# Kernel tuning notes

Measured on AMD Instinct MI355X. Metric: run time of the kernel, lower is better.

Reference implementation:

```python
import jax, jax.numpy as jnp
import numpy as np

EMBED_DIM = 768
HIDDEN_DIM = 384          # max(embed_dim // 2, 128)
NUM_HEADS = 12
HEAD_DIM = EMBED_DIM // NUM_HEADS
LAYER_VOCAB = 4           # len(target_layers)
THRESHOLD = 0.5
MIN_KEEP_RATIO = 0.1
B, N = 8, 1024


def setup_inputs() -> dict:
    key = jax.random.key(0)
    ks = jax.random.split(key, 12)
    std = 0.02
    return {
        "tokens": jax.random.normal(ks[0], (B, N, EMBED_DIM), jnp.float32),
        "layer_token_idx": 1,
        # actor params
        "layer_emb": jax.random.normal(ks[1], (LAYER_VOCAB, EMBED_DIM), jnp.float32) * std,
        "ln_g": jnp.ones((EMBED_DIM,), jnp.float32),
        "ln_b": jnp.zeros((EMBED_DIM,), jnp.float32),
        "w1": jax.random.normal(ks[2], (HIDDEN_DIM, EMBED_DIM), jnp.float32) * std,
        "b1": jnp.zeros((HIDDEN_DIM,), jnp.float32),
        "w2": jax.random.normal(ks[3], (HIDDEN_DIM, HIDDEN_DIM), jnp.float32) * std,
        "b2": jnp.zeros((HIDDEN_DIM,), jnp.float32),
        "w3": jax.random.normal(ks[4], (1, HIDDEN_DIM), jnp.float32) * std,
        "b3": jnp.zeros((1,), jnp.float32),
        # attention params (timm-style)
        "qkv_w": jax.random.normal(ks[5], (3 * EMBED_DIM, EMBED_DIM), jnp.float32) * std,
        "qkv_b": jnp.zeros((3 * EMBED_DIM,), jnp.float32),
        "proj_w": jax.random.normal(ks[6], (EMBED_DIM, EMBED_DIM), jnp.float32) * std,
        "proj_b": jnp.zeros((EMBED_DIM,), jnp.float32),
    }


def _layernorm(x, g, b, eps=1e-5):
    mu = x.mean(-1, keepdims=True)
    var = ((x - mu) ** 2).mean(-1, keepdims=True)
    return (x - mu) * jax.lax.rsqrt(var + eps) * g + b


def _forward(tokens, layer_token_idx, layer_emb, ln_g, ln_b, w1, b1, w2, b2, w3, b3,
             qkv_w, qkv_b, proj_w, proj_b):
    Bsz, Ntok, C = tokens.shape
    # --- MAPPOActor: logits ---
    ctx = tokens + layer_emb[layer_token_idx]               # broadcast [C]
    ctx = ctx + ctx.mean(axis=1, keepdims=True)             # global context
    h = _layernorm(ctx, ln_g, ln_b)
    h = jax.nn.gelu(h @ w1.T + b1, approximate=False)
    h = jax.nn.gelu(h @ w2.T + b2, approximate=False)
    logits = (h @ w3.T + b3).squeeze(-1)                    # [B, N]
    probs = jax.nn.sigmoid(logits)
    # --- compute_mask: threshold + min-keep topk correction ---
    binary = probs >= THRESHOLD                             # [B, N] bool
    min_keep = max(int(Ntok * MIN_KEEP_RATIO), 1)
    min_keep = min(min_keep, Ntok)
    _, topk_idx = jax.lax.top_k(probs, min_keep)            # [B, min_keep]
    fixed = jnp.zeros((Bsz, Ntok), bool).at[jnp.arange(Bsz)[:, None], topk_idx].set(True)
    need_fix = binary.sum(-1) < min_keep                    # [B]
    mask = jnp.where(need_fix[:, None], fixed, binary)
    mask = mask.at[:, 0].set(True)
    # --- masked attention (timm style) ---
    qkv = tokens @ qkv_w.T + qkv_b                          # [B, N, 3C]
    qkv = qkv.reshape(Bsz, Ntok, 3, NUM_HEADS, HEAD_DIM).transpose(2, 0, 3, 1, 4)
    q, k, v = qkv[0], qkv[1], qkv[2]                        # [B, H, N, D]
    q = q * (HEAD_DIM ** -0.5)
    scores = jnp.einsum("bhnd,bhmd->bhnm", q, k)            # [B, H, N, N]
    neg = jnp.finfo(scores.dtype).min
    scores = jnp.where(mask[:, None, None, :], scores, neg)
    attn = jax.nn.softmax(scores, axis=-1)
    v = v * mask[:, None, :, None].astype(v.dtype)
    out = jnp.einsum("bhnm,bhmd->bhnd", attn, v)
    out = out.transpose(0, 2, 1, 3).reshape(Bsz, Ntok, C)
    out = out @ proj_w.T + proj_b
    out = out * mask[..., None].astype(out.dtype)           # zero_out_queries=True
    return out


def reference(tokens, layer_token_idx, layer_emb, ln_g, ln_b, w1, b1, w2, b2, w3, b3,
              qkv_w, qkv_b, proj_w, proj_b):
    return _forward(tokens, layer_token_idx, layer_emb, ln_g, ln_b, w1, b1, w2, b2,
                    w3, b3, qkv_w, qkv_b, proj_w, proj_b)
```

## Files before the change

### kernel.cpp

```cpp
#include <hip/hip_runtime.h>
#include <cstdint>
#include <cmath>

#define EMBED 768
#define HID 384
#define NHEAD 12
#define HDIM 64
#define BATCH 8
#define NTOK 1024
#define MINKEEP 102

using f32x4  = __attribute__((ext_vector_type(4))) float;
using short8 = __attribute__((ext_vector_type(8))) short;
using short4v = __attribute__((ext_vector_type(4))) short;
using half8  = __attribute__((ext_vector_type(8))) _Float16;

__device__ inline short f2bf(float f) {
  unsigned u = __float_as_uint(f);
  u += 0x7fffu + ((u >> 16) & 1u);
  return (short)(u >> 16);
}
__device__ inline float bf2f(short s) {
  return __uint_as_float(((unsigned)(unsigned short)s) << 16);
}
__device__ inline unsigned pack_bf2(float lo, float hi) {
  unsigned ul = __float_as_uint(lo);
  ul += 0x7fffu + ((ul >> 16) & 1u);
  unsigned uh = __float_as_uint(hi);
  uh += 0x7fffu + ((uh >> 16) & 1u);
  return (ul >> 16) | (uh & 0xffff0000u);
}
__device__ inline void split2h(float v, short& h, short& m) {
  _Float16 h0 = (_Float16)v;
  float r = v - (float)h0;
  _Float16 m0 = (_Float16)r;
  h = __builtin_bit_cast(short, h0);
  m = __builtin_bit_cast(short, m0);
}

__global__ __launch_bounds__(256) void prep_kernel(
    const float* __restrict__ qkv_w, short* __restrict__ wq_bf,
    const float* __restrict__ proj_w, short* __restrict__ wp_bf,
    const float* __restrict__ w1, short* __restrict__ w1h, short* __restrict__ w1m,
    const float* __restrict__ w2, short* __restrict__ w2h, short* __restrict__ w2m,
    const float* __restrict__ tokens, float* __restrict__ colsum,
    float* __restrict__ lgt) {
  int blk = blockIdx.x, tid = threadIdx.x;
  if (blk < 2304) {
    const float* in = (blk < 1728) ? qkv_w : proj_w;
    short* out = (blk < 1728) ? wq_bf : wp_bf;
    int i = (blk < 1728 ? blk : blk - 1728) * 256 + tid;
    float4 f = ((const float4*)in)[i];
    short4v s;
    s[0] = f2bf(f.x); s[1] = f2bf(f.y); s[2] = f2bf(f.z); s[3] = f2bf(f.w);
    ((short4v*)out)[i] = s;
  } else if (blk < 2736) {
    const float* in = (blk < 2592) ? w1 : w2;
    short* oh = (blk < 2592) ? w1h : w2h;
    short* om = (blk < 2592) ? w1m : w2m;
    int i = (blk < 2592 ? blk - 2304 : blk - 2592) * 256 + tid;
    float4 f = ((const float4*)in)[i];
    short4v h, m;
    short th, tm;
    split2h(f.x, th, tm); h[0] = th; m[0] = tm;
    split2h(f.y, th, tm); h[1] = th; m[1] = tm;
    split2h(f.z, th, tm); h[2] = th; m[2] = tm;
    split2h(f.w, th, tm); h[3] = th; m[3] = tm;
    ((short4v*)oh)[i] = h;
    ((short4v*)om)[i] = m;
  } else if (blk < 2744) {
    int i = (blk - 2736) * 256 + tid;
    ((float4*)lgt)[i] = make_float4(0.f, 0.f, 0.f, 0.f);
  } else {
    int idx = blk - 2744;
    int b = idx >> 4, chunk = idx & 15;
    const float* tb = tokens + ((size_t)b * NTOK + chunk * 64) * EMBED;
    float s0 = 0.f, s1 = 0.f, s2 = 0.f;
#pragma unroll 8
    for (int n = 0; n < 64; ++n) {
      const float* r = tb + (size_t)n * EMBED;
      s0 += r[tid]; s1 += r[tid + 256]; s2 += r[tid + 512];
    }
    atomicAdd(&colsum[b * EMBED + tid], s0);
    atomicAdd(&colsum[b * EMBED + tid + 256], s1);
    atomicAdd(&colsum[b * EMBED + tid + 512], s2);
  }
}

__global__ __launch_bounds__(256) void ln_split_kernel(
    const float* __restrict__ tokens, const float* __restrict__ colsum,
    const float* __restrict__ layer_emb, const int* __restrict__ lidx,
    const float* __restrict__ gamma, const float* __restrict__ beta,
    short* __restrict__ xh, short* __restrict__ xm,
    short* __restrict__ tok_bf) {
  int row = blockIdx.x;
  int b = row >> 10;
  __shared__ float s_row[EMBED];
  __shared__ float s_red[4];
  const float* tr = tokens + (size_t)row * EMBED;
  const float* cs = colsum + b * EMBED;
  const float* eb = layer_emb + lidx[0] * EMBED;
  float lsum = 0.f;
  for (int c = threadIdx.x; c < EMBED; c += 256) {
    float t = tr[c];
    tok_bf[(size_t)row * EMBED + c] = f2bf(t);
    float v = t + 2.0f * eb[c] + cs[c] * (1.0f / NTOK);
    s_row[c] = v;
    lsum += v;
  }
  for (int o = 32; o; o >>= 1) lsum += __shfl_down(lsum, o, 64);
  int wid = threadIdx.x >> 6;
  if ((threadIdx.x & 63) == 0) s_red[wid] = lsum;
  __syncthreads();
  float mu = (s_red[0] + s_red[1] + s_red[2] + s_red[3]) * (1.f / EMBED);
  float lss = 0.f;
  for (int c = threadIdx.x; c < EMBED; c += 256) {
    float d = s_row[c] - mu;
    lss += d * d;
  }
  for (int o = 32; o; o >>= 1) lss += __shfl_down(lss, o, 64);
  __syncthreads();
  if ((threadIdx.x & 63) == 0) s_red[wid] = lss;
  __syncthreads();
  float var = (s_red[0] + s_red[1] + s_red[2] + s_red[3]) * (1.f / EMBED);
  float rinv = 1.0f / sqrtf(var + 1e-5f);
  for (int c = threadIdx.x; c < EMBED; c += 256) {
    float v = (s_row[c] - mu) * rinv * gamma[c] + beta[c];
    short h, m;
    split2h(v, h, m);
    size_t idx = (size_t)row * EMBED + c;
    xh[idx] = h; xm[idx] = m;
  }
}

__device__ inline float gelu_exact(float x) {
  return 0.5f * x * (1.0f + erff(x * 0.70710678118654752f));
}

template <int OUT>
__global__ __launch_bounds__(256) void gemm_split_kernel(
    const short* __restrict__ Ah, const short* __restrict__ Am,
    const short* __restrict__ Wh, const short* __restrict__ Wm,
    const float* __restrict__ bias, short* __restrict__ Ch,
    short* __restrict__ Cm, const float* __restrict__ w3,
    float* __restrict__ lgt, int M, int N, int K) {
  __shared__ short sA[2][64][40];
  __shared__ short sW[2][64][40];
  int tid = threadIdx.x;
  int w = tid >> 6, l = tid & 63, lg = l >> 4, lb = l & 15;
  int wr = (w >> 1) * 32, wc = (w & 1) * 32;
  int row0 = blockIdx.x * 64, col0 = blockIdx.y * 64;
  int srow = tid >> 2;
  int skk = (tid & 3) * 8;
  f32x4 acc0[2][2] = {}, acc1[2][2] = {};
  short8 ra0, ra1, rw0, rw1;
  {
    size_t aoff = (size_t)(row0 + srow) * K + skk;
    size_t woff = (size_t)(col0 + srow) * K + skk;
    ra0 = *(const short8*)(Ah + aoff);
    ra1 = *(const short8*)(Am + aoff);
    rw0 = *(const short8*)(Wh + woff);
    rw1 = *(const short8*)(Wm + woff);
  }
  for (int k0 = 0; k0 < K; k0 += 32) {
    __syncthreads();
    *(short8*)&sA[0][srow][skk] = ra0;
    *(short8*)&sA[1][srow][skk] = ra1;
    *(short8*)&sW[0][srow][skk] = rw0;
    *(short8*)&sW[1][srow][skk] = rw1;
    __syncthreads();
    if (k0 + 32 < K) {
      size_t aoff = (size_t)(row0 + srow) * K + k0 + 32 + skk;
      size_t woff = (size_t)(col0 + srow) * K + k0 + 32 + skk;
      ra0 = *(const short8*)(Ah + aoff);
      ra1 = *(const short8*)(Am + aoff);
      rw0 = *(const short8*)(Wh + woff);
      rw1 = *(const short8*)(Wm + woff);
    }
    half8 ah[2], am[2], bh[2], bm[2];
#pragma unroll
    for (int i = 0; i < 2; ++i) {
      ah[i] = *(half8*)&sA[0][wr + i * 16 + lb][lg * 8];
      am[i] = *(half8*)&sA[1][wr + i * 16 + lb][lg * 8];
      bh[i] = *(half8*)&sW[0][wc + i * 16 + lb][lg * 8];
      bm[i] = *(half8*)&sW[1][wc + i * 16 + lb][lg * 8];
    }
#pragma unroll
    for (int i = 0; i < 2; ++i)
#pragma unroll
      for (int j = 0; j < 2; ++j) {
        f32x4 c0 = acc0[i][j];
        f32x4 c1 = acc1[i][j];
        c0 = __builtin_amdgcn_mfma_f32_16x16x32_f16(ah[i], bh[j], c0, 0, 0, 0);
        c1 = __builtin_amdgcn_mfma_f32_16x16x32_f16(ah[i], bm[j], c1, 0, 0, 0);
        c0 = __builtin_amdgcn_mfma_f32_16x16x32_f16(am[i], bh[j], c0, 0, 0, 0);
        acc0[i][j] = c0;
        acc1[i][j] = c1;
      }
  }
  if (OUT == 0) {
#pragma unroll
    for (int i = 0; i < 2; ++i) {
#pragma unroll
      for (int j = 0; j < 2; ++j) {
#pragma unroll
        for (int r = 0; r < 4; ++r) {
          int grow = row0 + wr + i * 16 + lg * 4 + r;
          int gcol = col0 + wc + j * 16 + lb;
          float g = gelu_exact(acc0[i][j][r] + acc1[i][j][r] + bias[gcol]);
          size_t idx = (size_t)grow * N + gcol;
          short h, m;
          split2h(g, h, m);
          Ch[idx] = h; Cm[idx] = m;
        }
      }
    }
  } else {
    float part[2][4];
#pragma unroll
    for (int i = 0; i < 2; ++i)
#pragma unroll
      for (int r = 0; r < 4; ++r) part[i][r] = 0.f;
#pragma unroll
    for (int i = 0; i < 2; ++i) {
#pragma unroll
      for (int j = 0; j < 2; ++j) {
#pragma unroll
        for (int r = 0; r < 4; ++r) {
          int gcol = col0 + wc + j * 16 + lb;
          float g = gelu_exact(acc0[i][j][r] + acc1[i][j][r] + bias[gcol]);
          part[i][r] += g * w3[gcol];
        }
      }
    }
#pragma unroll
    for (int i = 0; i < 2; ++i) {
#pragma unroll
      for (int r = 0; r < 4; ++r) {
        float v = part[i][r];
        v += __shfl_xor(v, 1);
        v += __shfl_xor(v, 2);
        v += __shfl_xor(v, 4);
        v += __shfl_xor(v, 8);
        if (lb == 0) atomicAdd(&lgt[row0 + wr + i * 16 + lg * 4 + r], v);
      }
    }
  }
}

__global__ __launch_bounds__(1024) void mask_kernel(
    const float* __restrict__ lgt, const float* __restrict__ b3,
    int* __restrict__ kidx, int* __restrict__ kc, float* __restrict__ biasc) {
  int b = blockIdx.x, tid = threadIdx.x;
  __shared__ unsigned long long keys[1024];
  __shared__ int flag[1024];
  __shared__ int wsum[16];
  float v = lgt[b * NTOK + tid] + b3[0];
  bool bin = (v >= 0.0f);
  int wid = tid >> 6, lane = tid & 63;
  unsigned long long bal = __ballot(bin);
  if (lane == 0) wsum[wid] = __popcll(bal);
  __syncthreads();
  int total = 0;
  for (int q = 0; q < 16; ++q) total += wsum[q];
  int mv;
  if (total >= MINKEEP) {
    mv = bin ? 1 : 0;
  } else {
    flag[tid] = 0;
    unsigned u = __float_as_uint(v);
    u = (u & 0x80000000u) ? ~u : (u | 0x80000000u);
    keys[tid] = ((unsigned long long)u << 32) | (unsigned)(1023 - tid);
    __syncthreads();
    for (int k2 = 2; k2 <= 1024; k2 <<= 1) {
      for (int j = k2 >> 1; j > 0; j >>= 1) {
        int ixj = tid ^ j;
        if (ixj > tid) {
          unsigned long long a = keys[tid], c = keys[ixj];
          bool desc = ((tid & k2) == 0);
          if (desc ? (a < c) : (a > c)) {
            keys[tid] = c;
            keys[ixj] = a;
          }
        }
        __syncthreads();
      }
    }
    if (tid < MINKEEP) {
      int idx = 1023 - (int)(keys[tid] & 0xFFFFFFFFu);
      flag[idx] = 1;
    }
    __syncthreads();
    mv = flag[tid];
  }
  if (tid == 0) mv = 1;
  __syncthreads();
  unsigned long long fb = __ballot(mv != 0);
  if (lane == 0) wsum[wid] = __popcll(fb);
  __syncthreads();
  int base = 0, tot = 0;
  for (int q = 0; q < 16; ++q) {
    int vq = wsum[q];
    if (q < wid) base += vq;
    tot += vq;
  }
  if (mv) {
    int pre = base + __popcll(fb & ((1ull << lane) - 1ull));
    kidx[b * NTOK + pre] = tid;
    biasc[b * NTOK + pre] = 0.f;
  } else {
    int nbase = wid * 64 - base;
    int npre = nbase + __popcll(~fb & ((1ull << lane) - 1ull));
    kidx[b * NTOK + tot + npre] = tid;
    biasc[b * NTOK + tot + npre] = -3.0e38f;
  }
  if (tid == 0) kc[b] = tot;
}

__global__ __launch_bounds__(256) void qkv_gather_kernel(
    const short* __restrict__ tok_bf, const short* __restrict__ W,
    const float* __restrict__ bias, const int* __restrict__ kidx,
    const int* __restrict__ kc, short* __restrict__ qq,
    short* __restrict__ kk_, short* __restrict__ VTc) {
  __shared__ short smem[(64 + 128) * 72];
  short (*sA)[72] = (short(*)[72])smem;
  short (*sW)[72] = (short(*)[72])(smem + 64 * 72);
  __shared__ int s_idx[64];
  int bx = blockIdx.x;
  int b = bx & 7, bt = bx >> 3;
  int kcb = kc[b];
  if (bt * 64 >= kcb) return;
  int tid = threadIdx.x;
  if (tid < 64) s_idx[tid] = kidx[b * NTOK + bt * 64 + tid];
  int w = tid >> 6, l = tid & 63, lg = l >> 4, lb = l & 15;
  int wr = (w >> 1) * 32, wc = (w & 1) * 64;
  int col0 = blockIdx.y * 128;
  int r_ = tid >> 3, kq = (tid & 7) * 8;
  __syncthreads();
  const short* Ab = tok_bf + (size_t)b * NTOK * EMBED;
  f32x4 acc[2][4] = {};
  short8 pa[2], pw[4];
#pragma unroll
  for (int t = 0; t < 2; ++t)
    pa[t] = *(const short8*)(Ab + (size_t)s_idx[t * 32 + r_] * EMBED + kq);
#pragma unroll
  for (int t = 0; t < 4; ++t)
    pw[t] = *(const short8*)(W + (size_t)(col0 + t * 32 + r_) * EMBED + kq);
  for (int k0 = 0; k0 < EMBED; k0 += 64) {
    __syncthreads();
#pragma unroll
    for (int t = 0; t < 2; ++t) *(short8*)&sA[t * 32 + r_][kq] = pa[t];
#pragma unroll
    for (int t = 0; t < 4; ++t) *(short8*)&sW[t * 32 + r_][kq] = pw[t];
    __syncthreads();
    if (k0 + 64 < EMBED) {
#pragma unroll
      for (int t = 0; t < 2; ++t)
        pa[t] = *(const short8*)(Ab + (size_t)s_idx[t * 32 + r_] * EMBED +
                                 k0 + 64 + kq);
#pragma unroll
      for (int t = 0; t < 4; ++t)
        pw[t] = *(const short8*)(W + (size_t)(col0 + t * 32 + r_) * EMBED +
                                 k0 + 64 + kq);
    }
#pragma unroll
    for (int half = 0; half < 2; ++half) {
      short8 af[2], bfr[4];
#pragma unroll
      for (int i = 0; i < 2; ++i)
        af[i] = *(short8*)&sA[wr + i * 16 + lb][half * 32 + lg * 8];
#pragma unroll
      for (int j = 0; j < 4; ++j)
        bfr[j] = *(short8*)&sW[wc + j * 16 + lb][half * 32 + lg * 8];
#pragma unroll
      for (int i = 0; i < 2; ++i)
#pragma unroll
        for (int j = 0; j < 4; ++j)
          acc[i][j] = __builtin_amdgcn_mfma_f32_16x16x32_bf16(af[i], bfr[j],
                                                              acc[i][j], 0, 0, 0);
    }
  }
  if (col0 >= 2 * EMBED) {
    __syncthreads();
    short (*sT)[72] = (short(*)[72])smem;
#pragma unroll
    for (int i = 0; i < 2; ++i) {
#pragma unroll
      for (int j = 0; j < 4; ++j) {
        int col_local = wc + j * 16 + lb;
        int jr0 = wr + i * 16 + lg * 4;
        short4v v4;
#pragma unroll
        for (int r = 0; r < 4; ++r)
          v4[r] = f2bf(acc[i][j][r] + bias[col0 + col_local]);
        *(short4v*)&sT[col_local][jr0] = v4;
      }
    }
    __syncthreads();
    int rem = col0 - 2 * EMBED;
#pragma unroll
    for (int t = 0; t < 4; ++t) {
      int c = tid + t * 256;
      int rowl = c >> 3;
      int off = (c & 7) * 8;
      int vcol = rem + rowl;
      int h = vcol >> 6, d = vcol & 63;
      size_t dst = ((size_t)(b * NHEAD + h) * HDIM + d) * NTOK + bt * 64 + off;
      *(short8*)(VTc + dst) = *(short8*)&sT[rowl][off];
    }
    return;
  }
#pragma unroll
  for (int i = 0; i < 2; ++i) {
#pragma unroll
    for (int j = 0; j < 4; ++j) {
#pragma unroll
      for (int r = 0; r < 4; ++r) {
        int jrow = bt * 64 + wr + i * 16 + lg * 4 + r;
        int gcol = col0 + wc + j * 16 + lb;
        float val = acc[i][j][r] + bias[gcol];
        int which = gcol / EMBED;
        int rem2 = gcol - which * EMBED;
        int h = rem2 >> 6, d = rem2 & 63;
        size_t dst = ((size_t)(b * NHEAD + h) * NTOK + jrow) * HDIM + d;
        if (which == 0)
          qq[dst] = f2bf(val * 0.125f);
        else
          kk_[dst] = f2bf(val);
      }
    }
  }
}

#define ATTN_SWZ(row, colbyte) (((row)*128) + ((colbyte) ^ (((row)&7) << 4)))

__global__ __launch_bounds__(256) void attn_mfma3_kernel(
    const short* __restrict__ Qc, const short* __restrict__ Kc,
    const short* __restrict__ VTc, const float* __restrict__ biasc,
    const int* __restrict__ kc, short* __restrict__ ao) {
  __shared__ __align__(16) short sK[64 * 64];
  __shared__ __align__(16) short sVT[64 * 64];
  int bid = blockIdx.x;
  int xcd = bid & 7, slot = bid >> 3;
  int bh = xcd * 12 + (slot >> 4);
  int qt = slot & 15;
  int b = bh / NHEAD;
  int kcb = kc[b];
  if (qt * 64 >= kcb) return;
  int nt = (kcb + 63) >> 6;
  int tid = threadIdx.x;
  int w = tid >> 6, l = tid & 63, lg = l >> 4, lb = l & 15;
  int n0 = qt * 64 + w * 16;
  const short* Qp = Qc + ((size_t)bh * NTOK + n0) * HDIM;
  const short* Kp = Kc + (size_t)bh * NTOK * HDIM;
  const short* Vp = VTc + (size_t)bh * HDIM * NTOK;
  const float* bp = biasc + b * NTOK;

  short8 qf[2];
#pragma unroll
  for (int hh = 0; hh < 2; ++hh)
    qf[hh] = *(const short8*)(Qp + lb * HDIM + hh * 32 + lg * 8);

  f32x4 acc[4] = {};
  float lr = 0.f;

  int srow = tid >> 3;
  int scol = (tid & 7) * 8;
  int scolb = scol * 2;
  short8 rk0, rk1, rv0, rv1;

#define ATTN_LOADT(m0_)                                                        \
  {                                                                            \
    rk0 = *(const short8*)(Kp + (size_t)((m0_) + srow) * HDIM + scol);         \
    rk1 = *(const short8*)(Kp + (size_t)((m0_) + srow + 32) * HDIM + scol);    \
    rv0 = *(const short8*)(Vp + (size_t)srow * NTOK + (m0_) + scol);           \
    rv1 = *(const short8*)(Vp + (size_t)(srow + 32) * NTOK + (m0_) + scol);    \
  }

  ATTN_LOADT(0);
  for (int t = 0; t < nt; ++t) {
    int m0 = t * 64;
    *(short8*)((char*)sK + ATTN_SWZ(srow, scolb)) = rk0;
    *(short8*)((char*)sK + ATTN_SWZ(srow + 32, scolb)) = rk1;
    *(short8*)((char*)sVT + ATTN_SWZ(srow, scolb)) = rv0;
    *(short8*)((char*)sVT + ATTN_SWZ(srow + 32, scolb)) = rv1;
    __syncthreads();
    if (t + 1 < nt) ATTN_LOADT(m0 + 64);

    f32x4 bias4[4];
#pragma unroll
    for (int s = 0; s < 4; ++s)
      bias4[s] = *(const f32x4*)(bp + m0 + s * 16 + lg * 4);

    f32x4 S[4];
#pragma unroll
    for (int s = 0; s < 4; ++s) {
      short8 kf0 = *(const short8*)((const char*)sK +
                                    ATTN_SWZ(s * 16 + lb, lg * 16));
      short8 kf1 = *(const short8*)((const char*)sK +
                                    ATTN_SWZ(s * 16 + lb, 64 + lg * 16));
      f32x4 c = bias4[s];
      c = __builtin_amdgcn_mfma_f32_16x16x32_bf16(kf0, qf[0], c, 0, 0, 0);
      c = __builtin_amdgcn_mfma_f32_16x16x32_bf16(kf1, qf[1], c, 0, 0, 0);
      S[s] = c;
    }

    unsigned pk[4][2];
    {
      float rs = 0.f;
#pragma unroll
      for (int s = 0; s < 4; ++s) {
        float p0 = __expf(S[s][0]);
        float p1 = __expf(S[s][1]);
        float p2 = __expf(S[s][2]);
        float p3 = __expf(S[s][3]);
        rs += (p0 + p1) + (p2 + p3);
        pk[s][0] = pack_bf2(p0, p1);
        pk[s][1] = pack_bf2(p2, p3);
      }
      rs += __shfl_xor(rs, 16);
      rs += __shfl_xor(rs, 32);
      lr += rs;
    }

    bool hi = (lg & 2) != 0;
    int srcl = ((lg & 1) * 2) * 16 + lb;
#pragma unroll
    for (int t2 = 0; t2 < 2; ++t2) {
      short8 vf[4];
#pragma unroll
      for (int u = 0; u < 4; ++u)
        vf[u] = *(const short8*)((const char*)sVT +
                                 ATTN_SWZ(u * 16 + lb, t2 * 64 + lg * 16));
      int a0 = __shfl((int)pk[2 * t2][0], srcl);
      int b0 = __shfl((int)pk[2 * t2 + 1][0], srcl);
      int a1 = __shfl((int)pk[2 * t2][1], srcl);
      int b1 = __shfl((int)pk[2 * t2 + 1][1], srcl);
      int a2 = __shfl((int)pk[2 * t2][0], srcl + 16);
      int b2 = __shfl((int)pk[2 * t2 + 1][0], srcl + 16);
      int a3 = __shfl((int)pk[2 * t2][1], srcl + 16);
      int b3 = __shfl((int)pk[2 * t2 + 1][1], srcl + 16);
      union { short8 s8; int u[4]; } pa;
      pa.u[0] = hi ? b0 : a0;
      pa.u[1] = hi ? b1 : a1;
      pa.u[2] = hi ? b2 : a2;
      pa.u[3] = hi ? b3 : a3;
#pragma unroll
      for (int u = 0; u < 4; ++u)
        acc[u] = __builtin_amdgcn_mfma_f32_16x16x32_bf16(pa.s8, vf[u],
                                                         acc[u], 0, 0, 0);
    }
    __syncthreads();
  }

  int h = bh - b * NHEAD;
#pragma unroll
  for (int r = 0; r < 4; ++r) {
    float inv = 1.0f / __shfl(lr, lg * 4 + r);
    int j = n0 + lg * 4 + r;
#pragma unroll
    for (int u = 0; u < 4; ++u) {
      ao[((size_t)b * NTOK + j) * EMBED + h * HDIM + u * 16 + lb] =
          f2bf(acc[u][r] * inv);
    }
  }
}

__global__ __launch_bounds__(256) void proj_gather_kernel(
    const short* __restrict__ A, const short* __restrict__ W,
    const float* __restrict__ bias, const int* __restrict__ kidx,
    const int* __restrict__ kc, float* __restrict__ out) {
  __shared__ short sA[64][72];
  __shared__ short sW[128][72];
  __shared__ int s_idx[64];
  int bx = blockIdx.x;
  int b = bx & 7, bt = bx >> 3;
  int kcb = kc[b];
  int tid = threadIdx.x;
  if (tid < 64) s_idx[tid] = kidx[b * NTOK + bt * 64 + tid];
  int col0 = blockIdx.y * 128;
  if (bt * 64 >= kcb) {
    __syncthreads();
#pragma unroll
    for (int t = 0; t < 8; ++t) {
      int c = tid + t * 256;
      int rowl = c >> 5;
      int c4 = c & 31;
      int n = s_idx[rowl];
      ((float4*)(out + ((size_t)b * NTOK + n) * EMBED + col0))[c4] =
          make_float4(0.f, 0.f, 0.f, 0.f);
    }
    return;
  }
  int w = tid >> 6, l = tid & 63, lg = l >> 4, lb = l & 15;
  int wr = (w >> 1) * 32, wc = (w & 1) * 64;
  int r_ = tid >> 3, kq = (tid & 7) * 8;
  const short* Ab = A + ((size_t)b * NTOK + bt * 64) * EMBED;
  f32x4 acc[2][4] = {};
  short8 pa[2], pw[4];
  __syncthreads();
#pragma unroll
  for (int t = 0; t < 2; ++t)
    pa[t] = *(const short8*)(Ab + (size_t)(t * 32 + r_) * EMBED + kq);
#pragma unroll
  for (int t = 0; t < 4; ++t)
    pw[t] = *(const short8*)(W + (size_t)(col0 + t * 32 + r_) * EMBED + kq);
  for (int k0 = 0; k0 < EMBED; k0 += 64) {
    __syncthreads();
#pragma unroll
    for (int t = 0; t < 2; ++t) *(short8*)&sA[t * 32 + r_][kq] = pa[t];
#pragma unroll
    for (int t = 0; t < 4; ++t) *(short8*)&sW[t * 32 + r_][kq] = pw[t];
    __syncthreads();
    if (k0 + 64 < EMBED) {
#pragma unroll
      for (int t = 0; t < 2; ++t)
        pa[t] = *(const short8*)(Ab + (size_t)(t * 32 + r_) * EMBED + k0 + 64 + kq);
#pragma unroll
      for (int t = 0; t < 4; ++t)
        pw[t] = *(const short8*)(W + (size_t)(col0 + t * 32 + r_) * EMBED + k0 + 64 + kq);
    }
#pragma unroll
    for (int half = 0; half < 2; ++half) {
      short8 af[2], bfr[4];
#pragma unroll
      for (int i = 0; i < 2; ++i)
        af[i] = *(short8*)&sA[wr + i * 16 + lb][half * 32 + lg * 8];
#pragma unroll
      for (int j = 0; j < 4; ++j)
        bfr[j] = *(short8*)&sW[wc + j * 16 + lb][half * 32 + lg * 8];
#pragma unroll
      for (int i = 0; i < 2; ++i)
#pragma unroll
        for (int j = 0; j < 4; ++j)
          acc[i][j] = __builtin_amdgcn_mfma_f32_16x16x32_bf16(af[i], bfr[j],
                                                              acc[i][j], 0, 0, 0);
    }
  }
#pragma unroll
  for (int i = 0; i < 2; ++i) {
#pragma unroll
    for (int j = 0; j < 4; ++j) {
#pragma unroll
      for (int r = 0; r < 4; ++r) {
        int jloc = wr + i * 16 + lg * 4 + r;
        int jrow = bt * 64 + jloc;
        int gcol = col0 + wc + j * 16 + lb;
        int n = s_idx[jloc];
        out[((size_t)b * NTOK + n) * EMBED + gcol] =
            (jrow < kcb) ? (acc[i][j][r] + bias[gcol]) : 0.f;
      }
    }
  }
}

extern "C" void kernel_launch(void* const* d_in, const int* in_sizes, int n_in,
                              void* d_out, int out_size, void* d_ws, size_t ws_size,
                              hipStream_t stream) {
  const float* tokens   = (const float*)d_in[0];
  const int*   lidx     = (const int*)d_in[1];
  const float* layer_emb= (const float*)d_in[2];
  const float* ln_g     = (const float*)d_in[3];
  const float* ln_b     = (const float*)d_in[4];
  const float* w1       = (const float*)d_in[5];
  const float* b1       = (const float*)d_in[6];
  const float* w2       = (const float*)d_in[7];
  const float* b2       = (const float*)d_in[8];
  const float* w3       = (const float*)d_in[9];
  const float* b3       = (const float*)d_in[10];
  const float* qkv_w    = (const float*)d_in[11];
  const float* qkv_b    = (const float*)d_in[12];
  const float* proj_w   = (const float*)d_in[13];
  const float* proj_b   = (const float*)d_in[14];
  float* out = (float*)d_out;
  float* ws = (float*)d_ws;

  float* colsum = ws;
  float* lgt    = ws + 6144;
  int*   kidx   = (int*)(ws + 14336);
  float* biasc  = ws + 22528;
  int*   kc     = (int*)(ws + 30720);
  short* tok_bf = (short*)(ws + 30736);
  short* wq_bf  = (short*)(ws + 3176464);
  short* wp_bf  = (short*)(ws + 4061200);
  short* w1h = (short*)(ws + 4356112);
  short* w1m = (short*)(ws + 4503568);
  short* w2h = (short*)(ws + 4798480);
  short* w2m = (short*)(ws + 4872208);
  const size_t X0 = 5019664;
  short* xh  = (short*)(ws + X0);
  short* xm  = (short*)(ws + X0 + 3145728);
  short* h1h = (short*)(ws + X0 + 9437184);
  short* h1m = (short*)(ws + X0 + 11010048);
  short* Qc   = (short*)(ws + X0);
  short* Kc   = (short*)(ws + X0 + 3145728);
  short* VTc  = (short*)(ws + X0 + 9437184);
  short* aoc  = (short*)(ws + X0 + 12582912);

  hipMemsetAsync(colsum, 0, BATCH * EMBED * sizeof(float), stream);

  prep_kernel<<<dim3(2872), dim3(256), 0, stream>>>(
      qkv_w, wq_bf, proj_w, wp_bf, w1, w1h, w1m, w2, w2h, w2m,
      tokens, colsum, lgt);

  ln_split_kernel<<<dim3(BATCH * NTOK), dim3(256), 0, stream>>>(
      tokens, colsum, layer_emb, lidx, ln_g, ln_b, xh, xm, tok_bf);
  gemm_split_kernel<0><<<dim3(128, 6), dim3(256), 0, stream>>>(
      xh, xm, w1h, w1m, b1, h1h, h1m, nullptr, nullptr,
      BATCH * NTOK, HID, EMBED);
  gemm_split_kernel<1><<<dim3(128, 6), dim3(256), 0, stream>>>(
      h1h, h1m, w2h, w2m, b2, nullptr, nullptr, w3, lgt,
      BATCH * NTOK, HID, HID);
  mask_kernel<<<dim3(BATCH), dim3(1024), 0, stream>>>(lgt, b3, kidx, kc, biasc);

  qkv_gather_kernel<<<dim3(128, 18), dim3(256), 0, stream>>>(
      tok_bf, wq_bf, qkv_b, kidx, kc, Qc, Kc, VTc);
  attn_mfma3_kernel<<<dim3(1536), dim3(256), 0, stream>>>(
      Qc, Kc, VTc, biasc, kc, aoc);
  proj_gather_kernel<<<dim3(128, 6), dim3(256), 0, stream>>>(
      aoc, wp_bf, proj_b, kidx, kc, out);
}
```

Baseline: 150.5 us.

## Fuse mask computation into second MLP GEMM via last-block atomic counter

Removes the separate mask_kernel launch and performs thresholding, min-keep top-k sort and keep/drop compaction inside the tail of the second MLP GEMM. A per-batch atomic counter picks the last of 96 blocks covering that batch to run the mask logic with 256 threads, reusing the GEMM shared memory. This saves one kernel launch and its dependency gap. The cost is a threadfence and atomic in every block, plus a serialized 256-thread tail that does 4 tokens per thread.

```diff
diff --git a/kernel.cpp b/kernel.cpp
--- a/kernel.cpp
+++ b/kernel.cpp
@@ -44,7 +44,7 @@
     const float* __restrict__ w1, short* __restrict__ w1h, short* __restrict__ w1m,
     const float* __restrict__ w2, short* __restrict__ w2h, short* __restrict__ w2m,
     const float* __restrict__ tokens, float* __restrict__ colsum,
-    float* __restrict__ lgt) {
+    float* __restrict__ lgt, int* __restrict__ ctr) {
   int blk = blockIdx.x, tid = threadIdx.x;
   if (blk < 2304) {
     const float* in = (blk < 1728) ? qkv_w : proj_w;
@@ -71,6 +71,7 @@
   } else if (blk < 2744) {
     int i = (blk - 2736) * 256 + tid;
     ((float4*)lgt)[i] = make_float4(0.f, 0.f, 0.f, 0.f);
+    if (blk == 2736 && tid < BATCH) ctr[tid] = 0;
   } else {
     int idx = blk - 2744;
     int b = idx >> 4, chunk = idx & 15;
@@ -143,9 +144,12 @@
     const short* __restrict__ Wh, const short* __restrict__ Wm,
     const float* __restrict__ bias, short* __restrict__ Ch,
     short* __restrict__ Cm, const float* __restrict__ w3,
-    float* __restrict__ lgt, int M, int N, int K) {
-  __shared__ short sA[2][64][40];
-  __shared__ short sW[2][64][40];
+    float* __restrict__ lgt, const float* __restrict__ b3,
+    int* __restrict__ kidx, int* __restrict__ kcp,
+    float* __restrict__ biasc, int* __restrict__ ctr,
+    int M, int N, int K) {
+  __shared__ __align__(16) short sA[2][64][40];
+  __shared__ __align__(16) short sW[2][64][40];
   int tid = threadIdx.x;
   int w = tid >> 6, l = tid & 63, lg = l >> 4, lb = l & 15;
   int wr = (w >> 1) * 32, wc = (w & 1) * 32;
@@ -245,76 +249,100 @@
         if (lb == 0) atomicAdd(&lgt[row0 + wr + i * 16 + lg * 4 + r], v);
       }
     }
-  }
-}
-
-__global__ __launch_bounds__(1024) void mask_kernel(
-    const float* __restrict__ lgt, const float* __restrict__ b3,
-    int* __restrict__ kidx, int* __restrict__ kc, float* __restrict__ biasc) {
-  int b = blockIdx.x, tid = threadIdx.x;
-  __shared__ unsigned long long keys[1024];
-  __shared__ int flag[1024];
-  __shared__ int wsum[16];
-  float v = lgt[b * NTOK + tid] + b3[0];
-  bool bin = (v >= 0.0f);
-  int wid = tid >> 6, lane = tid & 63;
-  unsigned long long bal = __ballot(bin);
-  if (lane == 0) wsum[wid] = __popcll(bal);
-  __syncthreads();
-  int total = 0;
-  for (int q = 0; q < 16; ++q) total += wsum[q];
-  int mv;
-  if (total >= MINKEEP) {
-    mv = bin ? 1 : 0;
-  } else {
-    flag[tid] = 0;
-    unsigned u = __float_as_uint(v);
-    u = (u & 0x80000000u) ? ~u : (u | 0x80000000u);
-    keys[tid] = ((unsigned long long)u << 32) | (unsigned)(1023 - tid);
-    __syncthreads();
-    for (int k2 = 2; k2 <= 1024; k2 <<= 1) {
-      for (int j = k2 >> 1; j > 0; j >>= 1) {
-        int ixj = tid ^ j;
-        if (ixj > tid) {
-          unsigned long long a = keys[tid], c = keys[ixj];
-          bool desc = ((tid & k2) == 0);
-          if (desc ? (a < c) : (a > c)) {
-            keys[tid] = c;
-            keys[ixj] = a;
+    __threadfence();
+    __syncthreads();
+    __shared__ int s_last;
+    int b = row0 >> 10;
+    if (tid == 0) s_last = (atomicAdd(&ctr[b], 1) == 95) ? 1 : 0;
+    __syncthreads();
+    if (!s_last) return;
+    unsigned long long* keys = (unsigned long long*)&sA[0][0][0];
+    int* flags = (int*)&sW[0][0][0];
+    int* sscan = flags + 1024;
+    float b3v = b3[0];
+    float v4[4];
+    int mv[4];
+#pragma unroll
+    for (int t = 0; t < 4; ++t) {
+      v4[t] = atomicAdd(&lgt[b * NTOK + tid * 4 + t], 0.0f) + b3v;
+      mv[t] = (v4[t] >= 0.0f) ? 1 : 0;
+    }
+    int cnt = mv[0] + mv[1] + mv[2] + mv[3];
+    sscan[tid] = cnt;
+    __syncthreads();
+    for (int off = 128; off; off >>= 1) {
+      if (tid < off) sscan[tid] += sscan[tid + off];
+      __syncthreads();
+    }
+    int total = sscan[0];
+    __syncthreads();
+    if (total < MINKEEP) {
+#pragma unroll
+      for (int t = 0; t < 4; ++t) {
+        int tok = tid * 4 + t;
+        unsigned u = __float_as_uint(v4[t]);
+        u = (u & 0x80000000u) ? ~u : (u | 0x80000000u);
+        keys[tok] = ((unsigned long long)u << 32) | (unsigned)(1023 - tok);
+        flags[tok] = 0;
+      }
+      __syncthreads();
+      for (int k2 = 2; k2 <= 1024; k2 <<= 1) {
+        for (int j = k2 >> 1; j > 0; j >>= 1) {
+#pragma unroll
+          for (int t = 0; t < 4; ++t) {
+            int idx = tid + t * 256;
+            int ixj = idx ^ j;
+            if (ixj > idx) {
+              unsigned long long a = keys[idx], c = keys[ixj];
+              bool desc = ((idx & k2) == 0);
+              if (desc ? (a < c) : (a > c)) {
+                keys[idx] = c;
+                keys[ixj] = a;
+              }
+            }
           }
+          __syncthreads();
         }
-        __syncthreads();
-      }
-    }
-    if (tid < MINKEEP) {
-      int idx = 1023 - (int)(keys[tid] & 0xFFFFFFFFu);
-      flag[idx] = 1;
-    }
-    __syncthreads();
-    mv = flag[tid];
-  }
-  if (tid == 0) mv = 1;
-  __syncthreads();
-  unsigned long long fb = __ballot(mv != 0);
-  if (lane == 0) wsum[wid] = __popcll(fb);
-  __syncthreads();
-  int base = 0, tot = 0;
-  for (int q = 0; q < 16; ++q) {
-    int vq = wsum[q];
-    if (q < wid) base += vq;
-    tot += vq;
-  }
-  if (mv) {
-    int pre = base + __popcll(fb & ((1ull << lane) - 1ull));
-    kidx[b * NTOK + pre] = tid;
-    biasc[b * NTOK + pre] = 0.f;
-  } else {
-    int nbase = wid * 64 - base;
-    int npre = nbase + __popcll(~fb & ((1ull << lane) - 1ull));
-    kidx[b * NTOK + tot + npre] = tid;
-    biasc[b * NTOK + tot + npre] = -3.0e38f;
-  }
-  if (tid == 0) kc[b] = tot;
+      }
+#pragma unroll
+      for (int t = 0; t < 4; ++t) {
+        int idx = tid + t * 256;
+        if (idx < MINKEEP) flags[1023 - (int)(keys[idx] & 0xFFFFFFFFu)] = 1;
+      }
+      __syncthreads();
+#pragma unroll
+      for (int t = 0; t < 4; ++t) mv[t] = flags[tid * 4 + t];
+    }
+    if (tid == 0) mv[0] = 1;
+    int km = mv[0] + mv[1] + mv[2] + mv[3];
+    int bufsel = 0;
+    sscan[tid] = km;
+    __syncthreads();
+    for (int off = 1; off < 256; off <<= 1) {
+      int v2 = sscan[bufsel * 256 + tid] +
+               ((tid >= off) ? sscan[bufsel * 256 + tid - off] : 0);
+      sscan[(bufsel ^ 1) * 256 + tid] = v2;
+      bufsel ^= 1;
+      __syncthreads();
+    }
+    int incl = sscan[bufsel * 256 + tid];
+    int tot = sscan[bufsel * 256 + 255];
+    int kpre = incl - km;
+#pragma unroll
+    for (int t = 0; t < 4; ++t) {
+      int tok = tid * 4 + t;
+      if (mv[t]) {
+        kidx[b * NTOK + kpre] = tok;
+        biasc[b * NTOK + kpre] = 0.f;
+        ++kpre;
+      } else {
+        int cpos = tok - kpre;
+        kidx[b * NTOK + tot + cpos] = tok;
+        biasc[b * NTOK + tot + cpos] = -3.0e38f;
+      }
+    }
+    if (tid == 0) kcp[b] = tot;
+  }
 }
 
 __global__ __launch_bounds__(256) void qkv_gather_kernel(
@@ -680,6 +708,7 @@
   int*   kidx   = (int*)(ws + 14336);
   float* biasc  = ws + 22528;
   int*   kc     = (int*)(ws + 30720);
+  int*   ctr    = (int*)(ws + 30720) + 8;
   short* tok_bf = (short*)(ws + 30736);
   short* wq_bf  = (short*)(ws + 3176464);
   short* wp_bf  = (short*)(ws + 4061200);
@@ -701,17 +730,18 @@
 
   prep_kernel<<<dim3(2872), dim3(256), 0, stream>>>(
       qkv_w, wq_bf, proj_w, wp_bf, w1, w1h, w1m, w2, w2h, w2m,
-      tokens, colsum, lgt);
+      tokens, colsum, lgt, ctr);
 
   ln_split_kernel<<<dim3(BATCH * NTOK), dim3(256), 0, stream>>>(
       tokens, colsum, layer_emb, lidx, ln_g, ln_b, xh, xm, tok_bf);
   gemm_split_kernel<0><<<dim3(128, 6), dim3(256), 0, stream>>>(
       xh, xm, w1h, w1m, b1, h1h, h1m, nullptr, nullptr,
+      nullptr, nullptr, nullptr, nullptr, nullptr,
       BATCH * NTOK, HID, EMBED);
   gemm_split_kernel<1><<<dim3(128, 6), dim3(256), 0, stream>>>(
       h1h, h1m, w2h, w2m, b2, nullptr, nullptr, w3, lgt,
+      b3, kidx, kc, biasc, ctr,
       BATCH * NTOK, HID, HID);
-  mask_kernel<<<dim3(BATCH), dim3(1024), 0, stream>>>(lgt, b3, kidx, kc, biasc);
 
   qkv_gather_kernel<<<dim3(128, 18), dim3(256), 0, stream>>>(
       tok_bf, wq_bf, qkv_b, kidx, kc, Qc, Kc, VTc);
```

New measurement: 191.2 us. 27.1% more time.
